# Kernel optimization log

Measured on AMD Instinct MI355X. Metric: run time of the kernel, lower is better.

## Reference

```python
import jax, jax.numpy as jnp
import numpy as np

N = 50000
E = 800000
T = 10
H = 128
D = 64
P = 65536


def setup_inputs() -> dict:
    key = jax.random.key(0)
    ks = jax.random.split(key, 16)
    inp = {}
    inp["node_type_ids"] = jax.random.randint(ks[0], (N,), 0, T)
    inp["adj_rows"] = jax.random.randint(ks[1], (E,), 0, N)
    inp["adj_cols"] = jax.random.randint(ks[2], (E,), 0, N)
    inp["adj_vals"] = jax.random.uniform(ks[3], (E,), dtype=jnp.float32)
    inp["pairs"] = jax.random.randint(ks[4], (2, P), 0, N)
    s = 0.02
    inp["node_emb"] = jax.random.normal(ks[5], (N, H), dtype=jnp.float32) * s
    inp["type_emb"] = jax.random.normal(ks[6], (T, H), dtype=jnp.float32) * s
    inp["W1"] = jax.random.normal(ks[7], (H, H), dtype=jnp.float32) * s
    inp["b1"] = jnp.zeros((H,), dtype=jnp.float32)
    inp["W2"] = jax.random.normal(ks[8], (H, D), dtype=jnp.float32) * s
    inp["b2"] = jnp.zeros((D,), dtype=jnp.float32)
    inp["Wp1"] = jax.random.normal(ks[9], (3 * D, D), dtype=jnp.float32) * s
    inp["bp1"] = jnp.zeros((D,), dtype=jnp.float32)
    inp["Wp2"] = jax.random.normal(ks[10], (D, 1), dtype=jnp.float32) * s
    inp["bp2"] = jnp.zeros((1,), dtype=jnp.float32)
    return inp


def _spmm(rows, cols, vals, x):
    # sparse.mm(adj, x): out[r] = sum_e vals[e] * x[cols[e]] for rows[e]==r
    msgs = vals[:, None] * x[cols]          # [E, F] gather (irregular)
    return jax.ops.segment_sum(msgs, rows, num_segments=N)


def reference(node_type_ids, adj_rows, adj_cols, adj_vals, pairs,
              node_emb, type_emb, W1, b1, W2, b2, Wp1, bp1, Wp2, bp2):
    # encode: node_embedding(arange(N)) is just the full table
    x = node_emb + type_emb[node_type_ids]                    # [N, H]
    h = jax.nn.relu(_spmm(adj_rows, adj_cols, adj_vals, x) @ W1 + b1)  # gcn1 + relu
    # dropout is identity in eval mode
    z = _spmm(adj_rows, adj_cols, adj_vals, h) @ W2 + b2      # [N, D] gcn2
    # score
    src = z[pairs[0]]                                         # [P, D]
    dst = z[pairs[1]]                                         # [P, D]
    feat = jnp.concatenate([src, dst, src * dst], axis=-1)    # [P, 3D]
    out = jax.nn.relu(feat @ Wp1 + bp1) @ Wp2 + bp2           # [P, 1]
    return out[:, 0]
```

## Files before the change

kernel.cpp:

```cpp
#include <hip/hip_runtime.h>

#define N_NODES 50000
#define N_EDGES 800000
#define NPAIRS  65536

#define NBUCK 391
#define RTILE 2048
#define RBLOCKS 391

typedef unsigned short ushort_t;
typedef unsigned int uint_t;
typedef unsigned long long u64_t;
typedef ushort_t ushort8v __attribute__((ext_vector_type(8)));
typedef short bf16x8 __attribute__((ext_vector_type(8)));
typedef float f32x4 __attribute__((ext_vector_type(4)));

__device__ inline ushort_t f2bf(float f) {
    uint_t u = __float_as_uint(f);
    u = (u + 0x7FFF + ((u >> 16) & 1)) >> 16;
    return (ushort_t)u;
}
__device__ inline float bf2f(ushort_t b) {
    return __uint_as_float(((uint_t)b) << 16);
}


__global__ __launch_bounds__(256) void pack_hist_kernel(const int* __restrict__ rows,
                                                        const int* __restrict__ cols,
                                                        const float* __restrict__ vals,
                                                        u64_t* __restrict__ tmpA,
                                                        int* __restrict__ blockhist, int e) {
    __shared__ int lh[NBUCK];
    int blk = blockIdx.x, t = threadIdx.x;
    for (int i = t; i < NBUCK; i += 256) lh[i] = 0;
    __syncthreads();
    int base = blk * RTILE;
#pragma unroll
    for (int k = 0; k < RTILE / 256; k++) {
        int idx = base + k * 256 + t;
        if (idx < e) {
            int r = rows[idx];
            uint_t payload = (uint_t)cols[idx] | ((uint_t)f2bf(vals[idx]) << 16);
            tmpA[idx] = ((u64_t)r << 32) | payload;
            atomicAdd(&lh[r >> 7], 1);
        }
    }
    __syncthreads();
    for (int d = t; d < NBUCK; d += 256) blockhist[d * RBLOCKS + blk] = lh[d];
}

__global__ __launch_bounds__(256) void scan_block_kernel(const int* __restrict__ cnt,
                                                         int* __restrict__ excl,
                                                         int* __restrict__ blksum, int n) {
    __shared__ int s[256];
    int tid = threadIdx.x;
    int i = blockIdx.x * 256 + tid;
    int v = (i < n) ? cnt[i] : 0;
    s[tid] = v; __syncthreads();
    for (int off = 1; off < 256; off <<= 1) {
        int t = (tid >= off) ? s[tid - off] : 0;
        __syncthreads();
        s[tid] += t;
        __syncthreads();
    }
    if (i < n) excl[i] = s[tid] - v;
    if (tid == 255) blksum[blockIdx.x] = s[255];
}

__global__ __launch_bounds__(256) void scan_mid_kernel(int* __restrict__ data, int n) {
    __shared__ int s[256];
    __shared__ int carry;
    int t = threadIdx.x;
    if (t == 0) carry = 0;
    __syncthreads();
    for (int base = 0; base < n; base += 256) {
        int i = base + t;
        int v = (i < n) ? data[i] : 0;
        s[t] = v; __syncthreads();
        for (int off = 1; off < 256; off <<= 1) {
            int x = (t >= off) ? s[t - off] : 0;
            __syncthreads();
            s[t] += x;
            __syncthreads();
        }
        int excl = s[t] - v + carry;
        if (i < n) data[i] = excl;
        __syncthreads();
        if (t == 255) carry += s[255];
        __syncthreads();
    }
}

__global__ __launch_bounds__(256) void scan_add2_kernel(int* __restrict__ data,
                                                        const int* __restrict__ blksum, int n) {
    int i = blockIdx.x * 256 + threadIdx.x;
    if (i < n) data[i] += blksum[blockIdx.x];
}

__global__ __launch_bounds__(256) void radix_scatter_kernel(const u64_t* __restrict__ tmpA,
                                                            const int* __restrict__ gofs,
                                                            u64_t* __restrict__ tmpB, int e) {
    __shared__ u64_t stage[RTILE];
    __shared__ int lh[NBUCK];
    __shared__ int lstart[NBUCK];
    __shared__ int lcur[NBUCK];
    int blk = blockIdx.x, t = threadIdx.x;
    for (int i = t; i < NBUCK; i += 256) lh[i] = 0;
    __syncthreads();
    int base = blk * RTILE;
    int cnt = min(RTILE, e - base);
    for (int k = t; k < cnt; k += 256) {
        int d = (int)(tmpA[base + k] >> 39);
        atomicAdd(&lh[d], 1);
    }
    __syncthreads();
    if (t == 0) {
        int s = 0;
        for (int d = 0; d < NBUCK; d++) { lstart[d] = s; s += lh[d]; }
    }
    __syncthreads();
    for (int i = t; i < NBUCK; i += 256) lcur[i] = lstart[i];
    __syncthreads();
    for (int k = t; k < cnt; k += 256) {
        u64_t it = tmpA[base + k];
        int d = (int)(it >> 39);
        int slot = atomicAdd(&lcur[d], 1);
        stage[slot] = it;
    }
    __syncthreads();
    for (int k = t; k < cnt; k += 256) {
        u64_t it = stage[k];
        int d = (int)(it >> 39);
        tmpB[gofs[d * RBLOCKS + blk] + (k - lstart[d])] = it;
    }
}

__global__ __launch_bounds__(256) void bucket_sort_kernel(const u64_t* __restrict__ tmpB,
                                                          const int* __restrict__ gofs,
                                                          uint_t* __restrict__ csr_edge,
                                                          int* __restrict__ row_ptr, int e, int n) {
    __shared__ uint_t stage[4096];
    __shared__ int lh[128];
    __shared__ int lstart[128];
    __shared__ int lcur[128];
    int d = blockIdx.x, t = threadIdx.x;
    int bstart = gofs[d * RBLOCKS];
    int bend = (d == NBUCK - 1) ? e : gofs[(d + 1) * RBLOCKS];
    int len = bend - bstart;
    for (int i = t; i < 128; i += 256) lh[i] = 0;
    __syncthreads();
    for (int k = t; k < len; k += 256) {
        int lr = (int)((tmpB[bstart + k] >> 32) & 127);
        atomicAdd(&lh[lr], 1);
    }
    __syncthreads();
    if (t == 0) {
        int s = 0;
        for (int j = 0; j < 128; j++) { lstart[j] = s; s += lh[j]; }
    }
    __syncthreads();
    if (t < 128) {
        int grow = d * 128 + t;
        if (grow <= n) row_ptr[grow] = bstart + lstart[t];
    }
    for (int i = t; i < 128; i += 256) lcur[i] = lstart[i];
    __syncthreads();
    for (int k = t; k < len; k += 256) {
        u64_t it = tmpB[bstart + k];
        int lr = (int)((it >> 32) & 127);
        int slot = atomicAdd(&lcur[lr], 1);
        stage[slot] = (uint_t)it;
    }
    __syncthreads();
    for (int k = t; k < len; k += 256) csr_edge[bstart + k] = stage[k];
}


__global__ __launch_bounds__(256) void prep_w_kernel(const float* __restrict__ W1,
                                                     const float* __restrict__ W2,
                                                     const float* __restrict__ Wp1,
                                                     ushort_t* __restrict__ Wt1,
                                                     ushort_t* __restrict__ Wt2,
                                                     ushort_t* __restrict__ Wtp1) {
    int g = blockIdx.x * 256 + threadIdx.x;
    if (g < 2048) {
        int c = g & 127, k8 = g >> 7;
        ushort8v o;
#pragma unroll
        for (int j = 0; j < 8; j++) o[j] = f2bf(W1[(size_t)(k8 * 8 + j) * 128 + c]);
        *(ushort8v*)&Wt1[(size_t)c * 128 + k8 * 8] = o;
    } else if (g < 3072) {
        int g2 = g - 2048;
        int c = g2 & 63, k8 = g2 >> 6;
        ushort8v o;
#pragma unroll
        for (int j = 0; j < 8; j++) o[j] = f2bf(W2[(size_t)(k8 * 8 + j) * 64 + c]);
        *(ushort8v*)&Wt2[(size_t)c * 128 + k8 * 8] = o;
    } else if (g < 4608) {
        int g2 = g - 3072;
        int c = g2 / 24, k8 = g2 % 24;
        ushort8v o;
#pragma unroll
        for (int j = 0; j < 8; j++) o[j] = f2bf(Wp1[(size_t)(k8 * 8 + j) * 64 + c]);
        *(ushort8v*)&Wtp1[(size_t)g2 * 8] = o;
    }
}


__global__ __launch_bounds__(256) void gemm1_mfma_kernel(const float* __restrict__ node_emb,
                                                         const float* __restrict__ type_emb,
                                                         const int* __restrict__ tids,
                                                         const ushort_t* __restrict__ Wt1,
                                                         ushort_t* __restrict__ y, int n) {
    __shared__ __align__(16) ushort_t As[64 * 128];
    __shared__ __align__(16) ushort_t Ws[128 * 128];
    int t = threadIdx.x;

    for (int gi = t; gi < 2048; gi += 256) {
        int c = gi >> 4, kg = gi & 15;
        ushort8v v = *(const ushort8v*)&Wt1[gi * 8];
        *(ushort8v*)&Ws[c * 128 + ((kg ^ (c & 7)) << 3)] = v;
    }
    int row_l = t >> 2;
    int row_g = blockIdx.x * 64 + row_l;
    int kseg = (t & 3) * 32;
    if (row_g < n) {
        int tv = tids[row_g];
        const float4* na = (const float4*)(node_emb + (size_t)row_g * 128 + kseg);
        const float4* ta = (const float4*)(type_emb + (size_t)tv * 128 + kseg);
#pragma unroll
        for (int i2 = 0; i2 < 4; i2++) {
            float4 a = na[i2 * 2], b = ta[i2 * 2];
            float4 a2 = na[i2 * 2 + 1], b2 = ta[i2 * 2 + 1];
            ushort8v o;
            o[0] = f2bf(a.x + b.x);  o[1] = f2bf(a.y + b.y);
            o[2] = f2bf(a.z + b.z);  o[3] = f2bf(a.w + b.w);
            o[4] = f2bf(a2.x + b2.x); o[5] = f2bf(a2.y + b2.y);
            o[6] = f2bf(a2.z + b2.z); o[7] = f2bf(a2.w + b2.w);
            int kg = (t & 3) * 4 + i2;
            *(ushort8v*)&As[row_l * 128 + ((kg ^ (row_l & 7)) << 3)] = o;
        }
    } else {
        ushort8v z = (ushort8v)(ushort_t)0;
#pragma unroll
        for (int i2 = 0; i2 < 4; i2++) {
            int kg = (t & 3) * 4 + i2;
            *(ushort8v*)&As[row_l * 128 + ((kg ^ (row_l & 7)) << 3)] = z;
        }
    }
    __syncthreads();

    int lane = t & 63, wid = t >> 6;
    int m0 = (wid & 1) * 32, n0 = (wid >> 1) * 64;
    int lr = lane & 15, lk = lane >> 4;
    f32x4 acc[2][4] = {};
#pragma unroll
    for (int ks = 0; ks < 4; ks++) {
        int kg = ks * 4 + lk;
        bf16x8 afr[2];
#pragma unroll
        for (int mt = 0; mt < 2; mt++) {
            int r = m0 + mt * 16 + lr;
            afr[mt] = *(const bf16x8*)&As[r * 128 + ((kg ^ (r & 7)) << 3)];
        }
#pragma unroll
        for (int nt = 0; nt < 4; nt++) {
            int c = n0 + nt * 16 + lr;
            bf16x8 bfr = *(const bf16x8*)&Ws[c * 128 + ((kg ^ (c & 7)) << 3)];
            acc[0][nt] = __builtin_amdgcn_mfma_f32_16x16x32_bf16(afr[0], bfr, acc[0][nt], 0, 0, 0);
            acc[1][nt] = __builtin_amdgcn_mfma_f32_16x16x32_bf16(afr[1], bfr, acc[1][nt], 0, 0, 0);
        }
    }
#pragma unroll
    for (int mt = 0; mt < 2; mt++) {
#pragma unroll
        for (int j = 0; j < 4; j++) {
            int rg = blockIdx.x * 64 + m0 + mt * 16 + lk * 4 + j;
            if (rg < n) {
#pragma unroll
                for (int nt = 0; nt < 4; nt++) {
                    int c = n0 + nt * 16 + lr;
                    y[(size_t)rg * 128 + c] = f2bf(acc[mt][nt][j]);
                }
            }
        }
    }
}


__global__ __launch_bounds__(256) void gemm2_mfma_kernel(const ushort_t* __restrict__ h,
                                                         const ushort_t* __restrict__ Wt2,
                                                         ushort_t* __restrict__ g, int n) {
    __shared__ __align__(16) ushort_t As[64 * 128];
    __shared__ __align__(16) ushort_t Ws[64 * 128];
    int t = threadIdx.x;

    for (int gi = t; gi < 1024; gi += 256) {
        int c = gi >> 4, kg = gi & 15;
        ushort8v v = *(const ushort8v*)&Wt2[gi * 8];
        *(ushort8v*)&Ws[c * 128 + ((kg ^ (c & 7)) << 3)] = v;
    }
    int row_l = t >> 2;
    int row_g = blockIdx.x * 64 + row_l;
    int kseg = (t & 3) * 32;
    if (row_g < n) {
        const ushort8v* hr = (const ushort8v*)(h + (size_t)row_g * 128 + kseg);
#pragma unroll
        for (int i2 = 0; i2 < 4; i2++) {
            ushort8v v = hr[i2];
            int kg = (t & 3) * 4 + i2;
            *(ushort8v*)&As[row_l * 128 + ((kg ^ (row_l & 7)) << 3)] = v;
        }
    } else {
        ushort8v z = (ushort8v)(ushort_t)0;
#pragma unroll
        for (int i2 = 0; i2 < 4; i2++) {
            int kg = (t & 3) * 4 + i2;
            *(ushort8v*)&As[row_l * 128 + ((kg ^ (row_l & 7)) << 3)] = z;
        }
    }
    __syncthreads();

    int lane = t & 63, wid = t >> 6;
    int m0 = (wid & 1) * 32, n0 = (wid >> 1) * 32;
    int lr = lane & 15, lk = lane >> 4;
    f32x4 acc[2][2] = {};
#pragma unroll
    for (int ks = 0; ks < 4; ks++) {
        int kg = ks * 4 + lk;
        bf16x8 afr[2];
#pragma unroll
        for (int mt = 0; mt < 2; mt++) {
            int r = m0 + mt * 16 + lr;
            afr[mt] = *(const bf16x8*)&As[r * 128 + ((kg ^ (r & 7)) << 3)];
        }
#pragma unroll
        for (int nt = 0; nt < 2; nt++) {
            int c = n0 + nt * 16 + lr;
            bf16x8 bfr = *(const bf16x8*)&Ws[c * 128 + ((kg ^ (c & 7)) << 3)];
            acc[0][nt] = __builtin_amdgcn_mfma_f32_16x16x32_bf16(afr[0], bfr, acc[0][nt], 0, 0, 0);
            acc[1][nt] = __builtin_amdgcn_mfma_f32_16x16x32_bf16(afr[1], bfr, acc[1][nt], 0, 0, 0);
        }
    }
#pragma unroll
    for (int mt = 0; mt < 2; mt++) {
#pragma unroll
        for (int j = 0; j < 4; j++) {
            int rg = blockIdx.x * 64 + m0 + mt * 16 + lk * 4 + j;
            if (rg < n) {
#pragma unroll
                for (int nt = 0; nt < 2; nt++) {
                    int c = n0 + nt * 16 + lr;
                    g[(size_t)rg * 64 + c] = f2bf(acc[mt][nt][j]);
                }
            }
        }
    }
}


template <int F, bool RELU, bool BF16OUT>
__global__ __launch_bounds__(256) void spmm_v4_kernel(const int* __restrict__ row_ptr,
                                                      const uint_t* __restrict__ csr_edge,
                                                      const ushort_t* __restrict__ src,
                                                      const float* __restrict__ bias,
                                                      void* __restrict__ dst, int n) {
    constexpr int GL = F / 8;
    constexpr int RPB = (64 / GL) * 4;
    int t = threadIdx.x;
    int lane = t & 63, wid = t >> 6;
    int gl = lane % GL;
    int gbase = lane - gl;
    int row = blockIdx.x * RPB + wid * (64 / GL) + (lane / GL);
    int c8 = gl * 8;
    if (row >= n) return;
    int start = row_ptr[row], end = row_ptr[row + 1];

    float acc[8] = {};
    for (int base = start; base < end; base += GL) {
        int idx = base + gl;
        uint_t pe = (idx < end) ? csr_edge[idx] : 0u;
        int cnt = min(GL, end - base);
        for (int j = 0; j < cnt; j++) {
            uint_t p = (uint_t)__shfl((int)pe, gbase + j);
            int cc = p & 0xFFFF;
            float vv = bf2f((ushort_t)(p >> 16));
            const ushort8v s = *(const ushort8v*)(src + (size_t)cc * F + c8);
#pragma unroll
            for (int m = 0; m < 8; m++) acc[m] += vv * bf2f(s[m]);
        }
    }
#pragma unroll
    for (int m = 0; m < 8; m++) {
        acc[m] += bias[c8 + m];
        if (RELU) acc[m] = fmaxf(acc[m], 0.f);
    }
    if (BF16OUT) {
        ushort8v o;
#pragma unroll
        for (int m = 0; m < 8; m++) o[m] = f2bf(acc[m]);
        *(ushort8v*)((ushort_t*)dst + (size_t)row * F + c8) = o;
    } else {
        float4 o0 = make_float4(acc[0], acc[1], acc[2], acc[3]);
        float4 o1 = make_float4(acc[4], acc[5], acc[6], acc[7]);
        *(float4*)((float*)dst + (size_t)row * F + c8) = o0;
        *(float4*)((float*)dst + (size_t)row * F + c8 + 4) = o1;
    }
}


__global__ __launch_bounds__(256) void pair_mfma_kernel(const int* __restrict__ pairs,
                                                        const float* __restrict__ z,
                                                        const ushort_t* __restrict__ Wtp1,
                                                        const float* __restrict__ bp1,
                                                        const float* __restrict__ Wp2,
                                                        const float* __restrict__ bp2,
                                                        float* __restrict__ out) {
    __shared__ __align__(16) ushort_t Fs[64 * 192];
    __shared__ __align__(16) ushort_t Ws[64 * 192];
    int t = threadIdx.x;

    for (int gi = t; gi < 1536; gi += 256) {
        int c = gi / 24, kg = gi % 24;
        ushort8v v = *(const ushort8v*)&Wtp1[(size_t)gi * 8];
        *(ushort8v*)&Ws[c * 192 + ((kg ^ (c & 7)) << 3)] = v;
    }
    int row_l = t >> 2;
    int rg = blockIdx.x * 64 + row_l;
    int p0 = pairs[rg], p1 = pairs[NPAIRS + rg];
    const float* z0 = z + (size_t)p0 * 64;
    const float* z1 = z + (size_t)p1 * 64;
    int q = t & 3;
#pragma unroll
    for (int i = 0; i < 6; i++) {
        int kg = q * 6 + i;
        int k0 = kg * 8;
        float v[8];
        if (k0 < 64) {
#pragma unroll
            for (int m = 0; m < 8; m++) v[m] = z0[k0 + m];
        } else if (k0 < 128) {
#pragma unroll
            for (int m = 0; m < 8; m++) v[m] = z1[k0 - 64 + m];
        } else {
#pragma unroll
            for (int m = 0; m < 8; m++) v[m] = z0[k0 - 128 + m] * z1[k0 - 128 + m];
        }
        ushort8v o;
#pragma unroll
        for (int m = 0; m < 8; m++) o[m] = f2bf(v[m]);
        *(ushort8v*)&Fs[row_l * 192 + ((kg ^ (row_l & 7)) << 3)] = o;
    }
    __syncthreads();

    int lane = t & 63, wid = t >> 6;
    int m0 = wid * 16;
    int lr = lane & 15, lk = lane >> 4;
    f32x4 acc[4] = {};
#pragma unroll
    for (int ks = 0; ks < 6; ks++) {
        int kg = ks * 4 + lk;
        int r = m0 + lr;
        bf16x8 afr = *(const bf16x8*)&Fs[r * 192 + ((kg ^ (r & 7)) << 3)];
#pragma unroll
        for (int nt = 0; nt < 4; nt++) {
            int c = nt * 16 + lr;
            bf16x8 bfr = *(const bf16x8*)&Ws[c * 192 + ((kg ^ (c & 7)) << 3)];
            acc[nt] = __builtin_amdgcn_mfma_f32_16x16x32_bf16(afr, bfr, acc[nt], 0, 0, 0);
        }
    }
    float s[4] = {};
#pragma unroll
    for (int nt = 0; nt < 4; nt++) {
        int c = nt * 16 + lr;
        float b = bp1[c], w = Wp2[c];
#pragma unroll
        for (int j = 0; j < 4; j++) s[j] += fmaxf(acc[nt][j] + b, 0.f) * w;
    }
#pragma unroll
    for (int j = 0; j < 4; j++) {
        s[j] += __shfl_xor(s[j], 1);
        s[j] += __shfl_xor(s[j], 2);
        s[j] += __shfl_xor(s[j], 4);
        s[j] += __shfl_xor(s[j], 8);
    }
    if (lr == 0) {
        float bb = bp2[0];
#pragma unroll
        for (int j = 0; j < 4; j++)
            out[blockIdx.x * 64 + m0 + lk * 4 + j] = s[j] + bb;
    }
}


extern "C" void kernel_launch(void* const* d_in, const int* in_sizes, int n_in,
                              void* d_out, int out_size, void* d_ws, size_t ws_size,
                              hipStream_t stream) {
    const int*   tids     = (const int*)d_in[0];
    const int*   adj_rows = (const int*)d_in[1];
    const int*   adj_cols = (const int*)d_in[2];
    const float* adj_vals = (const float*)d_in[3];
    const int*   pairs    = (const int*)d_in[4];
    const float* node_emb = (const float*)d_in[5];
    const float* type_emb = (const float*)d_in[6];
    const float* W1  = (const float*)d_in[7];
    const float* b1  = (const float*)d_in[8];
    const float* W2  = (const float*)d_in[9];
    const float* b2  = (const float*)d_in[10];
    const float* Wp1 = (const float*)d_in[11];
    const float* bp1 = (const float*)d_in[12];
    const float* Wp2 = (const float*)d_in[13];
    const float* bp2 = (const float*)d_in[14];
    float* out = (float*)d_out;

    int n = in_sizes[0];
    int e = in_sizes[1];
    int p = in_sizes[4] / 2;

    char* ws = (char*)d_ws;
    ushort_t* bufY = (ushort_t*)ws;
    u64_t* tmpA = (u64_t*)ws;
    char* wsB = ws + (size_t)n * 128 * sizeof(ushort_t);
    ushort_t* bufH = (ushort_t*)wsB;
    float* bufZ = (float*)wsB;
    u64_t* tmpB = (u64_t*)wsB;

    int* row_ptr   = (int*)(wsB + (size_t)n * 128 * sizeof(ushort_t));
    int* blockhist = row_ptr + (n + 1);
    int L  = NBUCK * RBLOCKS;
    int* blksum1   = blockhist + L;
    uint_t* csr_edge = (uint_t*)(blksum1 + 1024);
    ushort_t* Wt1 = (ushort_t*)(csr_edge + e);
    ushort_t* Wt2 = Wt1 + 128 * 128;
    ushort_t* Wtp1 = Wt2 + 64 * 128;

    int SG = (L + 255) / 256;

    prep_w_kernel<<<18, 256, 0, stream>>>(W1, W2, Wp1, Wt1, Wt2, Wtp1);
    pack_hist_kernel<<<RBLOCKS, 256, 0, stream>>>(adj_rows, adj_cols, adj_vals, tmpA, blockhist, e);
    scan_block_kernel<<<SG, 256, 0, stream>>>(blockhist, blockhist, blksum1, L);
    scan_mid_kernel<<<1, 256, 0, stream>>>(blksum1, SG);
    scan_add2_kernel<<<SG, 256, 0, stream>>>(blockhist, blksum1, L);
    radix_scatter_kernel<<<RBLOCKS, 256, 0, stream>>>(tmpA, blockhist, tmpB, e);
    bucket_sort_kernel<<<NBUCK, 256, 0, stream>>>(tmpB, blockhist, csr_edge, row_ptr, e, n);

    gemm1_mfma_kernel<<<(n + 63) / 64, 256, 0, stream>>>(node_emb, type_emb, tids, Wt1, bufY, n);
    spmm_v4_kernel<128, true, true><<<(n + 15) / 16, 256, 0, stream>>>(row_ptr, csr_edge, bufY, b1, bufH, n);
    gemm2_mfma_kernel<<<(n + 63) / 64, 256, 0, stream>>>(bufH, Wt2, bufY, n);
    spmm_v4_kernel<64, false, false><<<(n + 31) / 32, 256, 0, stream>>>(row_ptr, csr_edge, bufY, b2, bufZ, n);
    pair_mfma_kernel<<<p / 64, 256, 0, stream>>>(pairs, bufZ, Wtp1, bp1, Wp2, bp2, out);
}
```

Baseline: 142.9 us.

## Split feature matrices into 32-column chunks so SpMM gathers hit cache

The GEMM outputs and SpMM inputs/outputs now use a chunked column-major layout: each 32-column slice of the node features is stored contiguously for all nodes. Each SpMM block handles one slice, so the random gather footprint per pass shrinks to 64 bytes per node and the per-chunk table fits in cache better. The cost is that adjacency row pointers and edges are re-read once per chunk, and the GEMM stores become more scattered.

```diff
diff --git a/kernel.cpp b/kernel.cpp
--- a/kernel.cpp
+++ b/kernel.cpp
@@ -280,7 +280,7 @@
 #pragma unroll
                 for (int nt = 0; nt < 4; nt++) {
                     int c = n0 + nt * 16 + lr;
-                    y[(size_t)rg * 128 + c] = f2bf(acc[mt][nt][j]);
+                    y[((size_t)(c >> 5) * n + rg) * 32 + (c & 31)] = f2bf(acc[mt][nt][j]);
                 }
             }
         }
@@ -302,20 +302,20 @@
     }
     int row_l = t >> 2;
     int row_g = blockIdx.x * 64 + row_l;
-    int kseg = (t & 3) * 32;
+    int ch = t & 3;
     if (row_g < n) {
-        const ushort8v* hr = (const ushort8v*)(h + (size_t)row_g * 128 + kseg);
+        const ushort8v* hr = (const ushort8v*)(h + ((size_t)ch * n + row_g) * 32);
 #pragma unroll
         for (int i2 = 0; i2 < 4; i2++) {
             ushort8v v = hr[i2];
-            int kg = (t & 3) * 4 + i2;
+            int kg = ch * 4 + i2;
             *(ushort8v*)&As[row_l * 128 + ((kg ^ (row_l & 7)) << 3)] = v;
         }
     } else {
         ushort8v z = (ushort8v)(ushort_t)0;
 #pragma unroll
         for (int i2 = 0; i2 < 4; i2++) {
-            int kg = (t & 3) * 4 + i2;
+            int kg = ch * 4 + i2;
             *(ushort8v*)&As[row_l * 128 + ((kg ^ (row_l & 7)) << 3)] = z;
         }
     }
@@ -351,7 +351,7 @@
 #pragma unroll
                 for (int nt = 0; nt < 2; nt++) {
                     int c = n0 + nt * 16 + lr;
-                    g[(size_t)rg * 64 + c] = f2bf(acc[mt][nt][j]);
+                    g[((size_t)(c >> 5) * n + rg) * 32 + (c & 31)] = f2bf(acc[mt][nt][j]);
                 }
             }
         }
@@ -359,52 +359,55 @@
 }
 
 
-template <int F, bool RELU, bool BF16OUT>
-__global__ __launch_bounds__(256) void spmm_v4_kernel(const int* __restrict__ row_ptr,
+template <int NCHUNK, bool RELU, bool BF16OUT>
+__global__ __launch_bounds__(256) void spmm_v5_kernel(const int* __restrict__ row_ptr,
                                                       const uint_t* __restrict__ csr_edge,
-                                                      const ushort_t* __restrict__ src,
+                                                      const ushort_t* __restrict__ src_base,
                                                       const float* __restrict__ bias,
                                                       void* __restrict__ dst, int n) {
-    constexpr int GL = F / 8;
-    constexpr int RPB = (64 / GL) * 4;
+    constexpr int SH = (NCHUNK == 4) ? 2 : 1;
+    int ch = blockIdx.x & (NCHUNK - 1);
+    int rowblk = blockIdx.x >> SH;
     int t = threadIdx.x;
     int lane = t & 63, wid = t >> 6;
-    int gl = lane % GL;
-    int gbase = lane - gl;
-    int row = blockIdx.x * RPB + wid * (64 / GL) + (lane / GL);
+    int gl = lane & 3;
+    int gbase = lane & ~3;
+    int row = rowblk * 64 + wid * 16 + (lane >> 2);
     int c8 = gl * 8;
     if (row >= n) return;
+    const ushort_t* src = src_base + (size_t)ch * n * 32;
     int start = row_ptr[row], end = row_ptr[row + 1];
 
     float acc[8] = {};
-    for (int base = start; base < end; base += GL) {
+    for (int base = start; base < end; base += 4) {
         int idx = base + gl;
         uint_t pe = (idx < end) ? csr_edge[idx] : 0u;
-        int cnt = min(GL, end - base);
+        int cnt = min(4, end - base);
         for (int j = 0; j < cnt; j++) {
             uint_t p = (uint_t)__shfl((int)pe, gbase + j);
             int cc = p & 0xFFFF;
             float vv = bf2f((ushort_t)(p >> 16));
-            const ushort8v s = *(const ushort8v*)(src + (size_t)cc * F + c8);
+            const ushort8v s = *(const ushort8v*)(src + (size_t)cc * 32 + c8);
 #pragma unroll
             for (int m = 0; m < 8; m++) acc[m] += vv * bf2f(s[m]);
         }
     }
+    int cg = ch * 32 + c8;
 #pragma unroll
     for (int m = 0; m < 8; m++) {
-        acc[m] += bias[c8 + m];
+        acc[m] += bias[cg + m];
         if (RELU) acc[m] = fmaxf(acc[m], 0.f);
     }
     if (BF16OUT) {
         ushort8v o;
 #pragma unroll
         for (int m = 0; m < 8; m++) o[m] = f2bf(acc[m]);
-        *(ushort8v*)((ushort_t*)dst + (size_t)row * F + c8) = o;
+        *(ushort8v*)((ushort_t*)dst + ((size_t)ch * n + row) * 32 + c8) = o;
     } else {
         float4 o0 = make_float4(acc[0], acc[1], acc[2], acc[3]);
         float4 o1 = make_float4(acc[4], acc[5], acc[6], acc[7]);
-        *(float4*)((float*)dst + (size_t)row * F + c8) = o0;
-        *(float4*)((float*)dst + (size_t)row * F + c8 + 4) = o1;
+        *(float4*)((float*)dst + (size_t)row * (NCHUNK * 32) + cg) = o0;
+        *(float4*)((float*)dst + (size_t)row * (NCHUNK * 32) + cg + 4) = o1;
     }
 }
 
@@ -544,9 +547,10 @@
     radix_scatter_kernel<<<RBLOCKS, 256, 0, stream>>>(tmpA, blockhist, tmpB, e);
     bucket_sort_kernel<<<NBUCK, 256, 0, stream>>>(tmpB, blockhist, csr_edge, row_ptr, e, n);
 
-    gemm1_mfma_kernel<<<(n + 63) / 64, 256, 0, stream>>>(node_emb, type_emb, tids, Wt1, bufY, n);
-    spmm_v4_kernel<128, true, true><<<(n + 15) / 16, 256, 0, stream>>>(row_ptr, csr_edge, bufY, b1, bufH, n);
-    gemm2_mfma_kernel<<<(n + 63) / 64, 256, 0, stream>>>(bufH, Wt2, bufY, n);
-    spmm_v4_kernel<64, false, false><<<(n + 31) / 32, 256, 0, stream>>>(row_ptr, csr_edge, bufY, b2, bufZ, n);
+    int rb = (n + 63) / 64;
+    gemm1_mfma_kernel<<<rb, 256, 0, stream>>>(node_emb, type_emb, tids, Wt1, bufY, n);
+    spmm_v5_kernel<4, true, true><<<rb * 4, 256, 0, stream>>>(row_ptr, csr_edge, bufY, b1, bufH, n);
+    gemm2_mfma_kernel<<<rb, 256, 0, stream>>>(bufH, Wt2, bufY, n);
+    spmm_v5_kernel<2, false, false><<<rb * 2, 256, 0, stream>>>(row_ptr, csr_edge, bufY, b2, bufZ, n);
     pair_mfma_kernel<<<p / 64, 256, 0, stream>>>(pairs, bufZ, Wtp1, bp1, Wp2, bp2, out);
 }
```

Result: no change. 144.9 us (+1.4%).

## Fuse weight prep into histogram, fold scan add, batch SpMM gathers

Applied to the files above, without the earlier changes.

The weight transpose/convert kernel is merged into the edge pack/histogram kernel as extra blocks, and the final scan-add pass is removed by having the scatter and bucket-sort kernels add the block sums themselves. Together these drop two launches. The SpMM inner loop now issues 8 or 4 neighbour-row gathers before accumulating, so several loads are in flight at once and gather latency is hidden. The cost is more registers per thread and a few extra global reads for the offsets.

```diff
diff --git a/kernel.cpp b/kernel.cpp
--- a/kernel.cpp
+++ b/kernel.cpp
@@ -25,13 +25,45 @@
 }
 
 
-__global__ __launch_bounds__(256) void pack_hist_kernel(const int* __restrict__ rows,
-                                                        const int* __restrict__ cols,
-                                                        const float* __restrict__ vals,
-                                                        u64_t* __restrict__ tmpA,
-                                                        int* __restrict__ blockhist, int e) {
+__global__ __launch_bounds__(256) void pack_hist_prep_kernel(const int* __restrict__ rows,
+                                                             const int* __restrict__ cols,
+                                                             const float* __restrict__ vals,
+                                                             u64_t* __restrict__ tmpA,
+                                                             int* __restrict__ blockhist, int e,
+                                                             const float* __restrict__ W1,
+                                                             const float* __restrict__ W2,
+                                                             const float* __restrict__ Wp1,
+                                                             ushort_t* __restrict__ Wt1,
+                                                             ushort_t* __restrict__ Wt2,
+                                                             ushort_t* __restrict__ Wtp1) {
+    int t = threadIdx.x;
+    if (blockIdx.x >= RBLOCKS) {
+        int g = (blockIdx.x - RBLOCKS) * 256 + t;
+        if (g < 2048) {
+            int c = g & 127, k8 = g >> 7;
+            ushort8v o;
+#pragma unroll
+            for (int j = 0; j < 8; j++) o[j] = f2bf(W1[(size_t)(k8 * 8 + j) * 128 + c]);
+            *(ushort8v*)&Wt1[(size_t)c * 128 + k8 * 8] = o;
+        } else if (g < 3072) {
+            int g2 = g - 2048;
+            int c = g2 & 63, k8 = g2 >> 6;
+            ushort8v o;
+#pragma unroll
+            for (int j = 0; j < 8; j++) o[j] = f2bf(W2[(size_t)(k8 * 8 + j) * 64 + c]);
+            *(ushort8v*)&Wt2[(size_t)c * 128 + k8 * 8] = o;
+        } else if (g < 4608) {
+            int g2 = g - 3072;
+            int c = g2 / 24, k8 = g2 % 24;
+            ushort8v o;
+#pragma unroll
+            for (int j = 0; j < 8; j++) o[j] = f2bf(Wp1[(size_t)(k8 * 8 + j) * 64 + c]);
+            *(ushort8v*)&Wtp1[(size_t)g2 * 8] = o;
+        }
+        return;
+    }
     __shared__ int lh[NBUCK];
-    int blk = blockIdx.x, t = threadIdx.x;
+    int blk = blockIdx.x;
     for (int i = t; i < NBUCK; i += 256) lh[i] = 0;
     __syncthreads();
     int base = blk * RTILE;
@@ -91,19 +123,16 @@
     }
 }
 
-__global__ __launch_bounds__(256) void scan_add2_kernel(int* __restrict__ data,
-                                                        const int* __restrict__ blksum, int n) {
-    int i = blockIdx.x * 256 + threadIdx.x;
-    if (i < n) data[i] += blksum[blockIdx.x];
-}
 
 __global__ __launch_bounds__(256) void radix_scatter_kernel(const u64_t* __restrict__ tmpA,
-                                                            const int* __restrict__ gofs,
+                                                            const int* __restrict__ blockhist,
+                                                            const int* __restrict__ blksum1,
                                                             u64_t* __restrict__ tmpB, int e) {
     __shared__ u64_t stage[RTILE];
     __shared__ int lh[NBUCK];
     __shared__ int lstart[NBUCK];
     __shared__ int lcur[NBUCK];
+    __shared__ int gstart[NBUCK];
     int blk = blockIdx.x, t = threadIdx.x;
     for (int i = t; i < NBUCK; i += 256) lh[i] = 0;
     __syncthreads();
@@ -119,7 +148,13 @@
         for (int d = 0; d < NBUCK; d++) { lstart[d] = s; s += lh[d]; }
     }
     __syncthreads();
-    for (int i = t; i < NBUCK; i += 256) lcur[i] = lstart[i];
+    for (int d = t; d < NBUCK; d += 256) {
+        lcur[d] = lstart[d];
+        if (lh[d]) {
+            int i = d * RBLOCKS + blk;
+            gstart[d] = blockhist[i] + blksum1[i >> 8];
+        }
+    }
     __syncthreads();
     for (int k = t; k < cnt; k += 256) {
         u64_t it = tmpA[base + k];
@@ -131,12 +166,13 @@
     for (int k = t; k < cnt; k += 256) {
         u64_t it = stage[k];
         int d = (int)(it >> 39);
-        tmpB[gofs[d * RBLOCKS + blk] + (k - lstart[d])] = it;
+        tmpB[gstart[d] + (k - lstart[d])] = it;
     }
 }
 
 __global__ __launch_bounds__(256) void bucket_sort_kernel(const u64_t* __restrict__ tmpB,
-                                                          const int* __restrict__ gofs,
+                                                          const int* __restrict__ blockhist,
+                                                          const int* __restrict__ blksum1,
                                                           uint_t* __restrict__ csr_edge,
                                                           int* __restrict__ row_ptr, int e, int n) {
     __shared__ uint_t stage[4096];
@@ -144,8 +180,14 @@
     __shared__ int lstart[128];
     __shared__ int lcur[128];
     int d = blockIdx.x, t = threadIdx.x;
-    int bstart = gofs[d * RBLOCKS];
-    int bend = (d == NBUCK - 1) ? e : gofs[(d + 1) * RBLOCKS];
+    int i0 = d * RBLOCKS;
+    int bstart = blockhist[i0] + blksum1[i0 >> 8];
+    int bend;
+    if (d == NBUCK - 1) bend = e;
+    else {
+        int i1 = (d + 1) * RBLOCKS;
+        bend = blockhist[i1] + blksum1[i1 >> 8];
+    }
     int len = bend - bstart;
     for (int i = t; i < 128; i += 256) lh[i] = 0;
     __syncthreads();
@@ -173,37 +215,6 @@
     }
     __syncthreads();
     for (int k = t; k < len; k += 256) csr_edge[bstart + k] = stage[k];
-}
-
-
-__global__ __launch_bounds__(256) void prep_w_kernel(const float* __restrict__ W1,
-                                                     const float* __restrict__ W2,
-                                                     const float* __restrict__ Wp1,
-                                                     ushort_t* __restrict__ Wt1,
-                                                     ushort_t* __restrict__ Wt2,
-                                                     ushort_t* __restrict__ Wtp1) {
-    int g = blockIdx.x * 256 + threadIdx.x;
-    if (g < 2048) {
-        int c = g & 127, k8 = g >> 7;
-        ushort8v o;
-#pragma unroll
-        for (int j = 0; j < 8; j++) o[j] = f2bf(W1[(size_t)(k8 * 8 + j) * 128 + c]);
-        *(ushort8v*)&Wt1[(size_t)c * 128 + k8 * 8] = o;
-    } else if (g < 3072) {
-        int g2 = g - 2048;
-        int c = g2 & 63, k8 = g2 >> 6;
-        ushort8v o;
-#pragma unroll
-        for (int j = 0; j < 8; j++) o[j] = f2bf(W2[(size_t)(k8 * 8 + j) * 64 + c]);
-        *(ushort8v*)&Wt2[(size_t)c * 128 + k8 * 8] = o;
-    } else if (g < 4608) {
-        int g2 = g - 3072;
-        int c = g2 / 24, k8 = g2 % 24;
-        ushort8v o;
-#pragma unroll
-        for (int j = 0; j < 8; j++) o[j] = f2bf(Wp1[(size_t)(k8 * 8 + j) * 64 + c]);
-        *(ushort8v*)&Wtp1[(size_t)g2 * 8] = o;
-    }
 }
 
 
@@ -360,7 +371,7 @@
 
 
 template <int F, bool RELU, bool BF16OUT>
-__global__ __launch_bounds__(256) void spmm_v4_kernel(const int* __restrict__ row_ptr,
+__global__ __launch_bounds__(256) void spmm_v7_kernel(const int* __restrict__ row_ptr,
                                                       const uint_t* __restrict__ csr_edge,
                                                       const ushort_t* __restrict__ src,
                                                       const float* __restrict__ bias,
@@ -381,7 +392,36 @@
         int idx = base + gl;
         uint_t pe = (idx < end) ? csr_edge[idx] : 0u;
         int cnt = min(GL, end - base);
-        for (int j = 0; j < cnt; j++) {
+        int j = 0;
+        for (; j + 8 <= cnt; j += 8) {
+            uint_t p[8];
+#pragma unroll
+            for (int u = 0; u < 8; u++) p[u] = (uint_t)__shfl((int)pe, gbase + j + u);
+            ushort8v s[8];
+#pragma unroll
+            for (int u = 0; u < 8; u++) s[u] = *(const ushort8v*)(src + (size_t)(p[u] & 0xFFFF) * F + c8);
+#pragma unroll
+            for (int u = 0; u < 8; u++) {
+                float vv = bf2f((ushort_t)(p[u] >> 16));
+#pragma unroll
+                for (int m = 0; m < 8; m++) acc[m] += vv * bf2f(s[u][m]);
+            }
+        }
+        for (; j + 4 <= cnt; j += 4) {
+            uint_t p[4];
+#pragma unroll
+            for (int u = 0; u < 4; u++) p[u] = (uint_t)__shfl((int)pe, gbase + j + u);
+            ushort8v s[4];
+#pragma unroll
+            for (int u = 0; u < 4; u++) s[u] = *(const ushort8v*)(src + (size_t)(p[u] & 0xFFFF) * F + c8);
+#pragma unroll
+            for (int u = 0; u < 4; u++) {
+                float vv = bf2f((ushort_t)(p[u] >> 16));
+#pragma unroll
+                for (int m = 0; m < 8; m++) acc[m] += vv * bf2f(s[u][m]);
+            }
+        }
+        for (; j < cnt; j++) {
             uint_t p = (uint_t)__shfl((int)pe, gbase + j);
             int cc = p & 0xFFFF;
             float vv = bf2f((ushort_t)(p >> 16));
@@ -536,17 +576,16 @@
 
     int SG = (L + 255) / 256;
 
-    prep_w_kernel<<<18, 256, 0, stream>>>(W1, W2, Wp1, Wt1, Wt2, Wtp1);
-    pack_hist_kernel<<<RBLOCKS, 256, 0, stream>>>(adj_rows, adj_cols, adj_vals, tmpA, blockhist, e);
+    pack_hist_prep_kernel<<<RBLOCKS + 18, 256, 0, stream>>>(adj_rows, adj_cols, adj_vals, tmpA, blockhist, e,
+                                                            W1, W2, Wp1, Wt1, Wt2, Wtp1);
     scan_block_kernel<<<SG, 256, 0, stream>>>(blockhist, blockhist, blksum1, L);
     scan_mid_kernel<<<1, 256, 0, stream>>>(blksum1, SG);
-    scan_add2_kernel<<<SG, 256, 0, stream>>>(blockhist, blksum1, L);
-    radix_scatter_kernel<<<RBLOCKS, 256, 0, stream>>>(tmpA, blockhist, tmpB, e);
-    bucket_sort_kernel<<<NBUCK, 256, 0, stream>>>(tmpB, blockhist, csr_edge, row_ptr, e, n);
+    radix_scatter_kernel<<<RBLOCKS, 256, 0, stream>>>(tmpA, blockhist, blksum1, tmpB, e);
+    bucket_sort_kernel<<<NBUCK, 256, 0, stream>>>(tmpB, blockhist, blksum1, csr_edge, row_ptr, e, n);
 
     gemm1_mfma_kernel<<<(n + 63) / 64, 256, 0, stream>>>(node_emb, type_emb, tids, Wt1, bufY, n);
-    spmm_v4_kernel<128, true, true><<<(n + 15) / 16, 256, 0, stream>>>(row_ptr, csr_edge, bufY, b1, bufH, n);
+    spmm_v7_kernel<128, true, true><<<(n + 15) / 16, 256, 0, stream>>>(row_ptr, csr_edge, bufY, b1, bufH, n);
     gemm2_mfma_kernel<<<(n + 63) / 64, 256, 0, stream>>>(bufH, Wt2, bufY, n);
-    spmm_v4_kernel<64, false, false><<<(n + 31) / 32, 256, 0, stream>>>(row_ptr, csr_edge, bufY, b2, bufZ, n);
+    spmm_v7_kernel<64, false, false><<<(n + 31) / 32, 256, 0, stream>>>(row_ptr, csr_edge, bufY, b2, bufZ, n);
     pair_mfma_kernel<<<p / 64, 256, 0, stream>>>(pairs, bufZ, Wtp1, bp1, Wp2, bp2, out);
 }
```

Measured after the change: 134.6 us. 1.06x faster.
